# Kernel tuning notes

Measured on AMD Instinct MI355X. Metric: run time of the kernel, lower is better.

The kernel has to match this reference:

```python
import jax, jax.numpy as jnp
import numpy as np

NEG = -1.0e9  # mask value used by apply_masking in the source


def setup_inputs() -> dict:
    key = jax.random.key(0)
    kq, kk, kv = jax.random.split(key, 3)
    B, H, S, Dh = 1, 16, 2048, 64
    q = jax.random.normal(kq, (B, H, S, Dh), dtype=jnp.float32)
    k = jax.random.normal(kk, (B, H, S, Dh), dtype=jnp.float32)
    v = jax.random.normal(kv, (B, H, S, Dh), dtype=jnp.float32)
    return {"q": q, "k": k, "v": v}


def reference(q, k, v):
    B, H, S, Dh = q.shape
    scaling = 1.0 / np.sqrt(Dh).astype(np.float32)
    # logits: [B,H,S,S]
    logits = jnp.einsum("bhqd,bhkd->bhqk", q, k) * scaling
    # causal mask: -1e9 strictly above diagonal (triu, diagonal=1)
    causal = jnp.where(
        jnp.triu(jnp.ones((S, S), dtype=bool), k=1), jnp.float32(NEG), jnp.float32(0.0)
    )[None, None]  # [1,1,S,S]
    z = jax.nn.sigmoid(logits) + causal
    log_beta = jax.nn.log_sigmoid(-logits) + causal
    # einsum('bhij,jk->bhik', log_beta, tril(ones)) == reverse cumsum over j
    re_cum_log_beta = jnp.flip(jnp.cumsum(jnp.flip(log_beta, -1), axis=-1), -1)
    weights = z * jnp.exp(re_cum_log_beta)
    return jnp.einsum("bhqk,bhkd->bhqd", weights, v)
```

## Files before the change

kernel.cpp:

```cpp
#include <hip/hip_runtime.h>
#include <math.h>

#define H 16
#define S 2048
#define D 64
#define NEED_WS (H * S * sizeof(float))

__device__ __forceinline__ float softplus_f(float x) {
    return fmaxf(x, 0.0f) + log1pf(expf(-fabsf(x)));
}

__global__ __launch_bounds__(256) void logits_kernel(const float* __restrict__ q,
                                                     const float* __restrict__ k,
                                                     float* __restrict__ ws_l)
{
    __shared__ float sQ[D];
    const int t = threadIdx.x;
    const int h = blockIdx.x >> 3;
    const int j = (blockIdx.x & 7) * 256 + t;

    const float* qh = q + ((size_t)h * S + (S - 1)) * D;
    if (t < D) sQ[t] = qh[t];
    __syncthreads();

    const float4* kr = (const float4*)(k + ((size_t)h * S + j) * D);
    float s = 0.f;
    #pragma unroll
    for (int x = 0; x < D / 4; ++x) {
        const float4 b = kr[x];
        s += sQ[4 * x + 0] * b.x + sQ[4 * x + 1] * b.y
           + sQ[4 * x + 2] * b.z + sQ[4 * x + 3] * b.w;
    }
    ws_l[(size_t)h * S + j] = s * 0.125f;
}

__global__ __launch_bounds__(256) void scan_gemv_kernel(const float* __restrict__ ws_l,
                                                        const float* __restrict__ v,
                                                        float* __restrict__ out)
{
    __shared__ float sS[257];
    __shared__ float sW[128];
    __shared__ float sRed[4][D];

    const int t  = threadIdx.x;
    const int h  = blockIdx.x >> 4;
    const int c  = blockIdx.x & 15;
    const int j0 = c * 128;
    const float* lrow = ws_l + (size_t)h * S;
    const float* vh   = v + (size_t)h * S * D;

    float lv[8], lb[8];
    {
        const float4 a = ((const float4*)(lrow + t * 8))[0];
        const float4 b = ((const float4*)(lrow + t * 8))[1];
        lv[0]=a.x; lv[1]=a.y; lv[2]=a.z; lv[3]=a.w;
        lv[4]=b.x; lv[5]=b.y; lv[6]=b.z; lv[7]=b.w;
    }
    float cs = 0.f;
    #pragma unroll
    for (int i = 0; i < 8; ++i) { lb[i] = -softplus_f(lv[i]); cs += lb[i]; }
    sS[t] = cs;
    if (t == 0) sS[256] = 0.f;
    __syncthreads();
    for (int off = 1; off < 256; off <<= 1) {
        const float x = sS[t] + ((t + off < 256) ? sS[t + off] : 0.f);
        __syncthreads();
        sS[t] = x;
        __syncthreads();
    }
    if ((t >> 4) == c) {
        float cr = sS[t + 1];
        float w[8];
        #pragma unroll
        for (int i = 7; i >= 0; --i) {
            cr += lb[i];
            w[i] = (1.f / (1.f + expf(-lv[i]))) * expf(cr);
        }
        const int base = t * 8 - j0;
        #pragma unroll
        for (int i = 0; i < 8; ++i) sW[base + i] = w[i];
    }
    __syncthreads();

    const int g = t >> 6;
    const int d = t & 63;
    float acc = 0.f;
    #pragma unroll 8
    for (int jj = g; jj < 128; jj += 4)
        acc += sW[jj] * vh[(size_t)(j0 + jj) * D + d];
    sRed[g][d] = acc;
    __syncthreads();
    if (g == 0) {
        const float tot = sRed[0][d] + sRed[1][d] + sRed[2][d] + sRed[3][d];
        atomicAdd(out + ((size_t)h * S + (S - 1)) * D + d, tot);
    }
}

__global__ __launch_bounds__(512) void sb_lastrow_kernel(const float* __restrict__ q,
                                                         const float* __restrict__ k,
                                                         const float* __restrict__ v,
                                                         float* __restrict__ out)
{
    __shared__ float sQ[D];
    __shared__ float sL[S];
    __shared__ float sS[513];
    __shared__ float sR[32][D + 4];

    const int t = threadIdx.x;
    const int h = blockIdx.x;
    const float* qh = q + ((size_t)h * S + (S - 1)) * D;
    const float* kh = k + (size_t)h * S * D;
    const float* vh = v + (size_t)h * S * D;

    if (t < D) sQ[t] = qh[t];
    __syncthreads();
    #pragma unroll
    for (int r = 0; r < S / 512; ++r) {
        const int j = t + r * 512;
        const float4* kr = (const float4*)(kh + (size_t)j * D);
        float s = 0.f;
        #pragma unroll
        for (int x = 0; x < D / 4; ++x) {
            const float4 b = kr[x];
            s += sQ[4*x+0]*b.x + sQ[4*x+1]*b.y + sQ[4*x+2]*b.z + sQ[4*x+3]*b.w;
        }
        sL[j] = s * 0.125f;
    }
    __syncthreads();
    float lv[4], lb[4];
    float cs = 0.f;
    #pragma unroll
    for (int i = 0; i < 4; ++i) {
        lv[i] = sL[t * 4 + i];
        lb[i] = -softplus_f(lv[i]);
        cs += lb[i];
    }
    sS[t] = cs;
    if (t == 0) sS[512] = 0.f;
    __syncthreads();
    for (int off = 1; off < 512; off <<= 1) {
        const float x = sS[t] + ((t + off < 512) ? sS[t + off] : 0.f);
        __syncthreads();
        sS[t] = x;
        __syncthreads();
    }
    float cr = sS[t + 1];
    #pragma unroll
    for (int i = 3; i >= 0; --i) {
        cr += lb[i];
        sL[t * 4 + i] = (1.f / (1.f + expf(-lv[i]))) * expf(cr);
    }
    __syncthreads();
    const int g  = t >> 4;
    const int c4 = t & 15;
    float4 acc = make_float4(0.f, 0.f, 0.f, 0.f);
    for (int j = g; j < S; j += 32) {
        const float w = sL[j];
        const float4 vv = ((const float4*)(vh + (size_t)j * D))[c4];
        acc.x += w*vv.x; acc.y += w*vv.y; acc.z += w*vv.z; acc.w += w*vv.w;
    }
    *((float4*)&sR[g][c4 * 4]) = acc;
    __syncthreads();
    for (int off = 16; off >= 1; off >>= 1) {
        if (g < off) {
            float4 a = *((float4*)&sR[g][c4 * 4]);
            const float4 b = *((float4*)&sR[g + off][c4 * 4]);
            a.x += b.x; a.y += b.y; a.z += b.z; a.w += b.w;
            *((float4*)&sR[g][c4 * 4]) = a;
        }
        __syncthreads();
    }
    if (g == 0)
        ((float4*)(out + ((size_t)h * S + (S - 1)) * D))[c4] = *((float4*)&sR[0][c4 * 4]);
}

extern "C" void kernel_launch(void* const* d_in, const int* in_sizes, int n_in,
                              void* d_out, int out_size, void* d_ws, size_t ws_size,
                              hipStream_t stream) {
    const float* q = (const float*)d_in[0];
    const float* k = (const float*)d_in[1];
    const float* v = (const float*)d_in[2];
    float* out = (float*)d_out;

    hipMemsetAsync(out, 0, (size_t)H * S * D * sizeof(float), stream);

    if (ws_size >= NEED_WS) {
        float* ws_l = (float*)d_ws;
        logits_kernel<<<dim3(H * 8), dim3(256), 0, stream>>>(q, k, ws_l);
        scan_gemv_kernel<<<dim3(H * 16), dim3(256), 0, stream>>>(ws_l, v, out);
    } else {
        sb_lastrow_kernel<<<dim3(H), dim3(512), 0, stream>>>(q, k, v, out);
    }
}
```

Before: 81.01 us.

## Fuse memset, logits and scan-gemv into one cooperative kernel with grid sync

```diff
diff --git a/kernel.cpp b/kernel.cpp
--- a/kernel.cpp
+++ b/kernel.cpp
@@ -1,5 +1,8 @@
 #include <hip/hip_runtime.h>
+#include <hip/hip_cooperative_groups.h>
 #include <math.h>
+
+namespace cg = cooperative_groups;
 
 #define H 16
 #define S 2048
@@ -10,41 +13,49 @@
     return fmaxf(x, 0.0f) + log1pf(expf(-fabsf(x)));
 }
 
-__global__ __launch_bounds__(256) void logits_kernel(const float* __restrict__ q,
-                                                     const float* __restrict__ k,
-                                                     float* __restrict__ ws_l)
+__global__ __launch_bounds__(256) void sb_fused_kernel(const float* __restrict__ q,
+                                                       const float* __restrict__ k,
+                                                       const float* __restrict__ v,
+                                                       float* __restrict__ out,
+                                                       float* __restrict__ ws_l)
 {
     __shared__ float sQ[D];
-    const int t = threadIdx.x;
-    const int h = blockIdx.x >> 3;
-    const int j = (blockIdx.x & 7) * 256 + t;
-
-    const float* qh = q + ((size_t)h * S + (S - 1)) * D;
-    if (t < D) sQ[t] = qh[t];
-    __syncthreads();
-
-    const float4* kr = (const float4*)(k + ((size_t)h * S + j) * D);
-    float s = 0.f;
-    #pragma unroll
-    for (int x = 0; x < D / 4; ++x) {
-        const float4 b = kr[x];
-        s += sQ[4 * x + 0] * b.x + sQ[4 * x + 1] * b.y
-           + sQ[4 * x + 2] * b.z + sQ[4 * x + 3] * b.w;
-    }
-    ws_l[(size_t)h * S + j] = s * 0.125f;
-}
-
-__global__ __launch_bounds__(256) void scan_gemv_kernel(const float* __restrict__ ws_l,
-                                                        const float* __restrict__ v,
-                                                        float* __restrict__ out)
-{
     __shared__ float sS[257];
     __shared__ float sW[128];
     __shared__ float sRed[4][D];
 
-    const int t  = threadIdx.x;
-    const int h  = blockIdx.x >> 4;
-    const int c  = blockIdx.x & 15;
+    const int t = threadIdx.x;
+    const int b = blockIdx.x;
+    const int gid = b * 256 + t;
+
+    {
+        float4* o4 = (float4*)out;
+        const float4 z = make_float4(0.f, 0.f, 0.f, 0.f);
+        #pragma unroll
+        for (int i = 0; i < 8; ++i) o4[gid + 65536 * i] = z;
+    }
+
+    if (b < 128) {
+        const int h = b >> 3;
+        const int j = (b & 7) * 256 + t;
+        const float* qh = q + ((size_t)h * S + (S - 1)) * D;
+        if (t < D) sQ[t] = qh[t];
+        __syncthreads();
+        const float4* kr = (const float4*)(k + ((size_t)h * S + j) * D);
+        float s = 0.f;
+        #pragma unroll
+        for (int x = 0; x < D / 4; ++x) {
+            const float4 bb = kr[x];
+            s += sQ[4 * x + 0] * bb.x + sQ[4 * x + 1] * bb.y
+               + sQ[4 * x + 2] * bb.z + sQ[4 * x + 3] * bb.w;
+        }
+        ws_l[(size_t)h * S + j] = s * 0.125f;
+    }
+
+    cg::this_grid().sync();
+
+    const int h  = b >> 4;
+    const int c  = b & 15;
     const int j0 = c * 128;
     const float* lrow = ws_l + (size_t)h * S;
     const float* vh   = v + (size_t)h * S * D;
@@ -52,9 +63,9 @@
     float lv[8], lb[8];
     {
         const float4 a = ((const float4*)(lrow + t * 8))[0];
-        const float4 b = ((const float4*)(lrow + t * 8))[1];
-        lv[0]=a.x; lv[1]=a.y; lv[2]=a.z; lv[3]=a.w;
-        lv[4]=b.x; lv[5]=b.y; lv[6]=b.z; lv[7]=b.w;
+        const float4 bb = ((const float4*)(lrow + t * 8))[1];
+        lv[0]=a.x;  lv[1]=a.y;  lv[2]=a.z;  lv[3]=a.w;
+        lv[4]=bb.x; lv[5]=bb.y; lv[6]=bb.z; lv[7]=bb.w;
     }
     float cs = 0.f;
     #pragma unroll
@@ -182,13 +193,13 @@
     const float* v = (const float*)d_in[2];
     float* out = (float*)d_out;
 
-    hipMemsetAsync(out, 0, (size_t)H * S * D * sizeof(float), stream);
-
     if (ws_size >= NEED_WS) {
         float* ws_l = (float*)d_ws;
-        logits_kernel<<<dim3(H * 8), dim3(256), 0, stream>>>(q, k, ws_l);
-        scan_gemv_kernel<<<dim3(H * 16), dim3(256), 0, stream>>>(ws_l, v, out);
+        void* args[] = {(void*)&q, (void*)&k, (void*)&v, (void*)&out, (void*)&ws_l};
+        hipLaunchCooperativeKernel((void*)sb_fused_kernel, dim3(256), dim3(256),
+                                   args, 0, stream);
     } else {
+        hipMemsetAsync(out, 0, (size_t)H * S * D * sizeof(float), stream);
         sb_lastrow_kernel<<<dim3(H), dim3(512), 0, stream>>>(q, k, v, out);
     }
 }
```

Measured after the change: 123.3 us. 52.2% more time.
